# Optimization experiments

Hardware: AMD Instinct MI355X
Metric: run time of the kernel (lower is better)

Reference implementation:

```python
import jax, jax.numpy as jnp
import numpy as np
from functools import partial

TOP_K = 2
LN_EPS = 1e-5


def setup_inputs() -> dict:
    key = jax.random.key(0)
    ks = jax.random.split(key, 4)
    B, T, H, F, E = 2, 2048, 1024, 4096, 8
    hidden_states = jax.random.normal(ks[0], (B, T, H), dtype=jnp.float32)
    # Router weights: original inits to zeros; use small random so routing is non-degenerate.
    router_w = jax.random.normal(ks[1], (E, H), dtype=jnp.float32) * 0.02
    router_b = jnp.zeros((E,), dtype=jnp.float32)
    W1 = jax.random.normal(ks[2], (E, H, F), dtype=jnp.float32) * (1.0 / np.sqrt(H))
    b1 = jnp.zeros((E, F), dtype=jnp.float32)
    W2 = jax.random.normal(ks[3], (E, F, H), dtype=jnp.float32) * (1.0 / np.sqrt(F))
    b2 = jnp.zeros((E, H), dtype=jnp.float32)
    ln_gamma = jnp.ones((H,), dtype=jnp.float32)
    ln_beta = jnp.zeros((H,), dtype=jnp.float32)
    return {"hidden_states": hidden_states, "router_w": router_w, "router_b": router_b,
            "W1": W1, "b1": b1, "W2": W2, "b2": b2,
            "ln_gamma": ln_gamma, "ln_beta": ln_beta}


def _layer_norm(x, gamma, beta):
    mu = jnp.mean(x, axis=-1, keepdims=True)
    var = jnp.var(x, axis=-1, keepdims=True)
    return (x - mu) * jax.lax.rsqrt(var + LN_EPS) * gamma + beta


def _moe_forward(hidden_states, router_w, router_b, W1, b1, W2, b2, ln_gamma, ln_beta):
    B, T, H = hidden_states.shape
    E = router_w.shape[0]
    N = B * T
    x = hidden_states.reshape(N, H)
    # Router (jitter=0.0, eval mode): logits [N, E]
    logits = x @ router_w.T + router_b
    topk_vals, topk_idx = jax.lax.top_k(logits, TOP_K)        # [N, K]
    topk_w = jax.nn.softmax(topk_vals, axis=-1)               # [N, K]
    # Scatter top-k weights into a dense combine matrix [N, E] (zeros elsewhere).
    probs = jnp.zeros((N, E), dtype=x.dtype).at[jnp.arange(N)[:, None], topk_idx].set(topk_w)
    # Per-expert FFN via scan over the (small, fixed) expert axis; each step is one
    # big GEMM over all tokens weighted by that expert's combine prob (0 for
    # tokens not routed to it) — same math as gather/MLP/scatter with no capacity drop.
    def body(acc, params_e):
        Wa, ba, Wb, bb, pe = params_e          # pe: [N]
        h = jax.nn.gelu(x @ Wa + ba, approximate=False)   # [N, F]
        y = h @ Wb + bb                                    # [N, H]
        return acc + y * pe[:, None], None
    out, _ = jax.lax.scan(body, jnp.zeros_like(x), (W1, b1, W2, b2, probs.T))
    out = out.reshape(B, T, H)
    return _layer_norm(out + hidden_states, ln_gamma, ln_beta)


def reference(hidden_states, router_w, router_b, W1, b1, W2, b2, ln_gamma, ln_beta):
    return _moe_forward(hidden_states, router_w, router_b, W1, b1, W2, b2, ln_gamma, ln_beta)
```

## Files before the change

kernel.cpp:

```cpp
#include <hip/hip_runtime.h>
#include <hip/hip_bf16.h>


typedef unsigned short u16;
typedef unsigned int u32;
typedef __attribute__((ext_vector_type(4))) float f32x4;
typedef __attribute__((ext_vector_type(8))) short s16x8;

#define GLD16(gp, lp) __builtin_amdgcn_global_load_lds( \
    (const __attribute__((address_space(1))) void*)(gp), \
    (__attribute__((address_space(3))) void*)(lp), 16, 0, 0)

__device__ __forceinline__ u16 f2bf(float f) {
    union { float f; u32 u; } v; v.f = f;
    u32 u = v.u;
    return (u16)((u + 0x7fffu + ((u >> 16) & 1u)) >> 16);
}

__global__ void k_init(int* cc) { if (threadIdx.x < 16) cc[threadIdx.x] = 0; }

__global__ __launch_bounds__(256) void k_router(
    const float* __restrict__ x, const float* __restrict__ rw, const float* __restrict__ rb,
    u16* __restrict__ xb, int* __restrict__ eidx, float* __restrict__ wgt, int* __restrict__ counts)
{
    const int wav = threadIdx.x >> 6, lane = threadIdx.x & 63;
    const int t = blockIdx.x * 4 + wav;
    const float* xt = x + (size_t)t * 1024;
    float acc[8] = {0.f,0.f,0.f,0.f,0.f,0.f,0.f,0.f};
    #pragma unroll
    for (int c = 0; c < 4; c++) {
        const int base = c * 256 + lane * 4;
        const float4 xv = *(const float4*)(xt + base);
        ushort4 pk;
        pk.x = f2bf(xv.x); pk.y = f2bf(xv.y); pk.z = f2bf(xv.z); pk.w = f2bf(xv.w);
        *(ushort4*)(xb + (size_t)t * 1024 + base) = pk;
        #pragma unroll
        for (int e = 0; e < 8; e++) {
            const float4 wv = *(const float4*)(rw + e * 1024 + base);
            acc[e] += xv.x * wv.x + xv.y * wv.y + xv.z * wv.z + xv.w * wv.w;
        }
    }
    #pragma unroll
    for (int e = 0; e < 8; e++) {
        #pragma unroll
        for (int s = 32; s; s >>= 1) acc[e] += __shfl_xor(acc[e], s);
    }
    if (lane == 0) {
        float v0 = -3e38f, v1 = -3e38f; int i0 = 0, i1 = 0;
        #pragma unroll
        for (int e = 0; e < 8; e++) {
            const float l = acc[e] + rb[e];
            if (l > v0) { v1 = v0; i1 = i0; v0 = l; i0 = e; }
            else if (l > v1) { v1 = l; i1 = e; }
        }
        const float w0 = 1.0f / (1.0f + expf(v1 - v0));
        eidx[2 * t] = i0; eidx[2 * t + 1] = i1;
        wgt[2 * t] = w0; wgt[2 * t + 1] = 1.0f - w0;
        atomicAdd(&counts[i0], 1); atomicAdd(&counts[i1], 1);
    }
}

__global__ void k_offsets(const int* __restrict__ counts, int* __restrict__ offsets) {
    if (threadIdx.x == 0) {
        int s = 0;
        for (int e = 0; e < 8; e++) { offsets[e] = s; s += counts[e]; }
        offsets[8] = s;
    }
}

__global__ __launch_bounds__(256) void k_place(
    const int* __restrict__ eidx, const int* __restrict__ offsets, int* __restrict__ cursors,
    int* __restrict__ rows, int* __restrict__ pos_of)
{
    const int a = blockIdx.x * 256 + threadIdx.x;
    const int e = eidx[a];
    const int pos = offsets[e] + atomicAdd(&cursors[e], 1);
    rows[pos] = a >> 1;
    pos_of[a] = pos;
}

__global__ __launch_bounds__(256) void k_transp(
    const float* __restrict__ src, u16* __restrict__ dst, int R, int C)
{
    __shared__ float tile[32][33];
    const int e = blockIdx.z;
    const float* s = src + (size_t)e * R * C;
    u16* d = dst + (size_t)e * R * C;
    const int c0 = blockIdx.x * 32, r0 = blockIdx.y * 32;
    const int tx = threadIdx.x & 31, ty = threadIdx.x >> 5;
    #pragma unroll
    for (int j = 0; j < 4; j++)
        tile[ty * 4 + j][tx] = s[(size_t)(r0 + ty * 4 + j) * C + c0 + tx];
    __syncthreads();
    #pragma unroll
    for (int j = 0; j < 4; j++)
        d[(size_t)(c0 + ty * 4 + j) * R + r0 + tx] = f2bf(tile[tx][ty * 4 + j]);
}

__global__ __launch_bounds__(256) void k_gemm1(
    const u16* __restrict__ xb, const u16* __restrict__ W1t, const float* __restrict__ b1,
    u16* __restrict__ hbuf, const int* __restrict__ rows, const int* __restrict__ offsets)
{
    const int e = blockIdx.z;
    const int off = offsets[e], cnt = offsets[e + 1] - off;
    const int row0 = blockIdx.y * 128;
    if (row0 >= cnt) return;
    const int n0 = blockIdx.x * 128;
    const int tid = threadIdx.x;
    const int lane = tid & 63, wav = tid >> 6;

    __shared__ u16 At[128][32];
    __shared__ u16 Bt[128][32];

    const int ar0 = tid >> 2, ar1 = ar0 + 64;
    const int cl8 = (tid & 3) * 8;
    const int t0 = rows[off + min(row0 + ar0, cnt - 1)];
    const int t1 = rows[off + min(row0 + ar1, cnt - 1)];
    const u16* a_src0 = xb + (size_t)t0 * 1024 + cl8;
    const u16* a_src1 = xb + (size_t)t1 * 1024 + cl8;
    const u16* b_src0 = W1t + ((size_t)e * 4096 + n0 + ar0) * 1024 + cl8;
    const u16* b_src1 = W1t + ((size_t)e * 4096 + n0 + ar1) * 1024 + cl8;

    char* a_d0 = (char*)At + wav * 1024;
    char* a_d1 = (char*)At + 4096 + wav * 1024;
    char* b_d0 = (char*)Bt + wav * 1024;
    char* b_d1 = (char*)Bt + 4096 + wav * 1024;

    f32x4 acc[4][4] = {};
    const int wr = wav >> 1, wc = wav & 1;
    const int koff = (lane >> 4) * 8;
    const u16* Ab = &At[wr * 64 + (lane & 15)][koff];
    const u16* Bb = &Bt[wc * 64 + (lane & 15)][koff];

    for (int k0 = 0; k0 < 1024; k0 += 32) {
        GLD16(a_src0 + k0, a_d0);
        GLD16(a_src1 + k0, a_d1);
        GLD16(b_src0 + k0, b_d0);
        GLD16(b_src1 + k0, b_d1);
        __syncthreads();
        s16x8 af[4], bfr[4];
        #pragma unroll
        for (int i = 0; i < 4; i++) {
            af[i]  = *(const s16x8*)(Ab + i * 512);
            bfr[i] = *(const s16x8*)(Bb + i * 512);
        }
        #pragma unroll
        for (int mi = 0; mi < 4; mi++)
            #pragma unroll
            for (int ni = 0; ni < 4; ni++)
                acc[mi][ni] = __builtin_amdgcn_mfma_f32_16x16x32_bf16(af[mi], bfr[ni], acc[mi][ni], 0, 0, 0);
        __syncthreads();
    }

    const int rb4 = (lane >> 4) * 4;
    #pragma unroll
    for (int mi = 0; mi < 4; mi++) {
        #pragma unroll
        for (int j = 0; j < 4; j++) {
            const int lrow = wr * 64 + mi * 16 + rb4 + j;
            if (row0 + lrow < cnt) {
                const size_t gr = (size_t)(off + row0 + lrow);
                #pragma unroll
                for (int ni = 0; ni < 4; ni++) {
                    const int col = n0 + wc * 64 + ni * 16 + (lane & 15);
                    const float v = acc[mi][ni][j] + b1[e * 4096 + col];
                    const float g = 0.5f * v * (1.0f + erff(v * 0.70710678118654752f));
                    hbuf[gr * 4096 + col] = f2bf(g);
                }
            }
        }
    }
}

__global__ __launch_bounds__(256) void k_gemm2(
    const u16* __restrict__ hbuf, const u16* __restrict__ W2t, const float* __restrict__ b2,
    float* __restrict__ y, const int* __restrict__ offsets)
{
    const int e = blockIdx.z;
    const int off = offsets[e], cnt = offsets[e + 1] - off;
    const int row0 = blockIdx.y * 128;
    if (row0 >= cnt) return;
    const int n0 = blockIdx.x * 128;
    const int tid = threadIdx.x;
    const int lane = tid & 63, wav = tid >> 6;

    __shared__ u16 At[128][32];
    __shared__ u16 Bt[128][32];

    const int ar0 = tid >> 2, ar1 = ar0 + 64;
    const int cl8 = (tid & 3) * 8;
    const u16* a_src0 = hbuf + (size_t)(off + min(row0 + ar0, cnt - 1)) * 4096 + cl8;
    const u16* a_src1 = hbuf + (size_t)(off + min(row0 + ar1, cnt - 1)) * 4096 + cl8;
    const u16* b_src0 = W2t + ((size_t)e * 1024 + n0 + ar0) * 4096 + cl8;
    const u16* b_src1 = W2t + ((size_t)e * 1024 + n0 + ar1) * 4096 + cl8;

    char* a_d0 = (char*)At + wav * 1024;
    char* a_d1 = (char*)At + 4096 + wav * 1024;
    char* b_d0 = (char*)Bt + wav * 1024;
    char* b_d1 = (char*)Bt + 4096 + wav * 1024;

    f32x4 acc[4][4] = {};
    const int wr = wav >> 1, wc = wav & 1;
    const int koff = (lane >> 4) * 8;
    const u16* Ab = &At[wr * 64 + (lane & 15)][koff];
    const u16* Bb = &Bt[wc * 64 + (lane & 15)][koff];

    for (int k0 = 0; k0 < 4096; k0 += 32) {
        GLD16(a_src0 + k0, a_d0);
        GLD16(a_src1 + k0, a_d1);
        GLD16(b_src0 + k0, b_d0);
        GLD16(b_src1 + k0, b_d1);
        __syncthreads();
        s16x8 af[4], bfr[4];
        #pragma unroll
        for (int i = 0; i < 4; i++) {
            af[i]  = *(const s16x8*)(Ab + i * 512);
            bfr[i] = *(const s16x8*)(Bb + i * 512);
        }
        #pragma unroll
        for (int mi = 0; mi < 4; mi++)
            #pragma unroll
            for (int ni = 0; ni < 4; ni++)
                acc[mi][ni] = __builtin_amdgcn_mfma_f32_16x16x32_bf16(af[mi], bfr[ni], acc[mi][ni], 0, 0, 0);
        __syncthreads();
    }

    const int rb4 = (lane >> 4) * 4;
    #pragma unroll
    for (int mi = 0; mi < 4; mi++) {
        #pragma unroll
        for (int j = 0; j < 4; j++) {
            const int lrow = wr * 64 + mi * 16 + rb4 + j;
            if (row0 + lrow < cnt) {
                const size_t gr = (size_t)(off + row0 + lrow);
                #pragma unroll
                for (int ni = 0; ni < 4; ni++) {
                    const int col = n0 + wc * 64 + ni * 16 + (lane & 15);
                    y[gr * 1024 + col] = acc[mi][ni][j] + b2[e * 1024 + col];
                }
            }
        }
    }
}

__global__ __launch_bounds__(256) void k_combine(
    const float* __restrict__ x, const float* __restrict__ y,
    const int* __restrict__ pos_of, const float* __restrict__ wgt,
    const float* __restrict__ gamma, const float* __restrict__ beta,
    float* __restrict__ out)
{
    const int t = blockIdx.x;
    const int tid = threadIdx.x;
    const int p0 = pos_of[2 * t], p1 = pos_of[2 * t + 1];
    const float w0 = wgt[2 * t], w1 = wgt[2 * t + 1];
    const int j4 = tid * 4;
    const float4 xv = *(const float4*)(x + (size_t)t * 1024 + j4);
    const float4 y0 = *(const float4*)(y + (size_t)p0 * 1024 + j4);
    const float4 y1 = *(const float4*)(y + (size_t)p1 * 1024 + j4);
    float a0 = xv.x + w0 * y0.x + w1 * y1.x;
    float a1 = xv.y + w0 * y0.y + w1 * y1.y;
    float a2 = xv.z + w0 * y0.z + w1 * y1.z;
    float a3 = xv.w + w0 * y0.w + w1 * y1.w;
    float s = a0 + a1 + a2 + a3;
    float q = a0 * a0 + a1 * a1 + a2 * a2 + a3 * a3;
    #pragma unroll
    for (int o = 32; o; o >>= 1) { s += __shfl_xor(s, o); q += __shfl_xor(q, o); }
    __shared__ float ls[4], lq[4];
    const int wav = tid >> 6, lane = tid & 63;
    if (lane == 0) { ls[wav] = s; lq[wav] = q; }
    __syncthreads();
    s = ls[0] + ls[1] + ls[2] + ls[3];
    q = lq[0] + lq[1] + lq[2] + lq[3];
    const float mu = s * (1.0f / 1024.0f);
    const float var = q * (1.0f / 1024.0f) - mu * mu;
    const float rs = rsqrtf(var + 1e-5f);
    const float4 g = *(const float4*)(gamma + j4);
    const float4 b = *(const float4*)(beta + j4);
    float4 o4;
    o4.x = (a0 - mu) * rs * g.x + b.x;
    o4.y = (a1 - mu) * rs * g.y + b.y;
    o4.z = (a2 - mu) * rs * g.z + b.z;
    o4.w = (a3 - mu) * rs * g.w + b.w;
    *(float4*)(out + (size_t)t * 1024 + j4) = o4;
}

extern "C" void kernel_launch(void* const* d_in, const int* in_sizes, int n_in,
                              void* d_out, int out_size, void* d_ws, size_t ws_size,
                              hipStream_t stream) {
    const float* x     = (const float*)d_in[0];
    const float* rw    = (const float*)d_in[1];
    const float* rb    = (const float*)d_in[2];
    const float* W1    = (const float*)d_in[3];
    const float* b1    = (const float*)d_in[4];
    const float* W2    = (const float*)d_in[5];
    const float* b2    = (const float*)d_in[6];
    const float* gamma = (const float*)d_in[7];
    const float* beta  = (const float*)d_in[8];
    float* out = (float*)d_out;

    char* p = (char*)d_ws;
    auto alloc = [&](size_t bytes) { char* r = p; p += (bytes + 255) & ~(size_t)255; return r; };
    int*   counts  = (int*)alloc(16 * sizeof(int));
    int*   cursors = counts + 8;
    int*   offsets = (int*)alloc(9 * sizeof(int));
    int*   eidx    = (int*)alloc(8192 * sizeof(int));
    float* wgt     = (float*)alloc(8192 * sizeof(float));
    int*   pos_of  = (int*)alloc(8192 * sizeof(int));
    int*   rows    = (int*)alloc(8192 * sizeof(int));
    u16*   xb      = (u16*)alloc((size_t)4096 * 1024 * 2);
    u16*   W1t     = (u16*)alloc((size_t)8 * 4096 * 1024 * 2);
    u16*   W2t     = (u16*)alloc((size_t)8 * 1024 * 4096 * 2);
    u16*   hbuf    = (u16*)alloc((size_t)8192 * 4096 * 2);
    float* y       = (float*)alloc((size_t)8192 * 1024 * 4);

    hipLaunchKernelGGL(k_init, dim3(1), dim3(64), 0, stream, counts);
    hipLaunchKernelGGL(k_router, dim3(1024), dim3(256), 0, stream, x, rw, rb, xb, eidx, wgt, counts);
    hipLaunchKernelGGL(k_offsets, dim3(1), dim3(64), 0, stream, counts, offsets);
    hipLaunchKernelGGL(k_place, dim3(32), dim3(256), 0, stream, eidx, offsets, cursors, rows, pos_of);
    hipLaunchKernelGGL(k_transp, dim3(128, 32, 8), dim3(256), 0, stream, W1, W1t, 1024, 4096);
    hipLaunchKernelGGL(k_transp, dim3(32, 128, 8), dim3(256), 0, stream, W2, W2t, 4096, 1024);
    hipLaunchKernelGGL(k_gemm1, dim3(32, 32, 8), dim3(256), 0, stream, xb, W1t, b1, hbuf, rows, offsets);
    hipLaunchKernelGGL(k_gemm2, dim3(8, 32, 8), dim3(256), 0, stream, hbuf, W2t, b2, y, offsets);
    hipLaunchKernelGGL(k_combine, dim3(4096), dim3(256), 0, stream, x, y, pos_of, wgt, gamma, beta, out);
}
```

Measured before the change: 502.2 us.

## Split-K gemm2, tanh GELU, and vectorized weight transpose

Splits the second expert GEMM into two K halves, writing partial outputs into buffers that reuse the dead W1t storage, and sums them in the combine kernel. This raises block-level parallelism. The exact erf GELU is replaced by a tanh-style approximation built from fast exp and rcp. The transpose kernel drops LDS tiling and has each thread gather 8 rows and store them with one 16-byte write. The approximate GELU introduces small numeric deviation from the exact reference.

```diff
diff --git a/kernel.cpp b/kernel.cpp
--- a/kernel.cpp
+++ b/kernel.cpp
@@ -6,6 +6,7 @@
 typedef unsigned int u32;
 typedef __attribute__((ext_vector_type(4))) float f32x4;
 typedef __attribute__((ext_vector_type(8))) short s16x8;
+typedef __attribute__((ext_vector_type(8))) unsigned short u16x8;
 
 #define GLD16(gp, lp) __builtin_amdgcn_global_load_lds( \
     (const __attribute__((address_space(1))) void*)(gp), \
@@ -15,6 +16,12 @@
     union { float f; u32 u; } v; v.f = f;
     u32 u = v.u;
     return (u16)((u + 0x7fffu + ((u >> 16) & 1u)) >> 16);
+}
+
+__device__ __forceinline__ float gelu_f(float v) {
+    const float u = v * (0.7978845608f + 0.0356774081f * v * v);
+    const float t = __expf(-2.0f * u);
+    return v * __builtin_amdgcn_rcpf(1.0f + t);
 }
 
 __global__ void k_init(int* cc) { if (threadIdx.x < 16) cc[threadIdx.x] = 0; }
@@ -82,19 +89,16 @@
 __global__ __launch_bounds__(256) void k_transp(
     const float* __restrict__ src, u16* __restrict__ dst, int R, int C)
 {
-    __shared__ float tile[32][33];
     const int e = blockIdx.z;
     const float* s = src + (size_t)e * R * C;
     u16* d = dst + (size_t)e * R * C;
-    const int c0 = blockIdx.x * 32, r0 = blockIdx.y * 32;
-    const int tx = threadIdx.x & 31, ty = threadIdx.x >> 5;
-    #pragma unroll
-    for (int j = 0; j < 4; j++)
-        tile[ty * 4 + j][tx] = s[(size_t)(r0 + ty * 4 + j) * C + c0 + tx];
-    __syncthreads();
-    #pragma unroll
-    for (int j = 0; j < 4; j++)
-        d[(size_t)(c0 + ty * 4 + j) * R + r0 + tx] = f2bf(tile[tx][ty * 4 + j]);
+    const int c = blockIdx.x * 64 + (threadIdx.x >> 2);
+    const int r0 = blockIdx.y * 32 + (threadIdx.x & 3) * 8;
+    u16x8 v;
+    #pragma unroll
+    for (int k = 0; k < 8; k++)
+        v[k] = f2bf(s[(size_t)(r0 + k) * C + c]);
+    *(u16x8*)(d + (size_t)c * R + r0) = v;
 }
 
 __global__ __launch_bounds__(256) void k_gemm1(
@@ -164,8 +168,7 @@
                 for (int ni = 0; ni < 4; ni++) {
                     const int col = n0 + wc * 64 + ni * 16 + (lane & 15);
                     const float v = acc[mi][ni][j] + b1[e * 4096 + col];
-                    const float g = 0.5f * v * (1.0f + erff(v * 0.70710678118654752f));
-                    hbuf[gr * 4096 + col] = f2bf(g);
+                    hbuf[gr * 4096 + col] = f2bf(gelu_f(v));
                 }
             }
         }
@@ -174,25 +177,26 @@
 
 __global__ __launch_bounds__(256) void k_gemm2(
     const u16* __restrict__ hbuf, const u16* __restrict__ W2t, const float* __restrict__ b2,
-    float* __restrict__ y, const int* __restrict__ offsets)
-{
-    const int e = blockIdx.z;
+    float* __restrict__ y0, float* __restrict__ y1, const int* __restrict__ offsets)
+{
+    const int e = blockIdx.z >> 1, kh = blockIdx.z & 1;
     const int off = offsets[e], cnt = offsets[e + 1] - off;
     const int row0 = blockIdx.y * 128;
     if (row0 >= cnt) return;
     const int n0 = blockIdx.x * 128;
     const int tid = threadIdx.x;
     const int lane = tid & 63, wav = tid >> 6;
+    const int kbase = kh * 2048;
 
     __shared__ u16 At[128][32];
     __shared__ u16 Bt[128][32];
 
     const int ar0 = tid >> 2, ar1 = ar0 + 64;
     const int cl8 = (tid & 3) * 8;
-    const u16* a_src0 = hbuf + (size_t)(off + min(row0 + ar0, cnt - 1)) * 4096 + cl8;
-    const u16* a_src1 = hbuf + (size_t)(off + min(row0 + ar1, cnt - 1)) * 4096 + cl8;
-    const u16* b_src0 = W2t + ((size_t)e * 1024 + n0 + ar0) * 4096 + cl8;
-    const u16* b_src1 = W2t + ((size_t)e * 1024 + n0 + ar1) * 4096 + cl8;
+    const u16* a_src0 = hbuf + (size_t)(off + min(row0 + ar0, cnt - 1)) * 4096 + kbase + cl8;
+    const u16* a_src1 = hbuf + (size_t)(off + min(row0 + ar1, cnt - 1)) * 4096 + kbase + cl8;
+    const u16* b_src0 = W2t + ((size_t)e * 1024 + n0 + ar0) * 4096 + kbase + cl8;
+    const u16* b_src1 = W2t + ((size_t)e * 1024 + n0 + ar1) * 4096 + kbase + cl8;
 
     char* a_d0 = (char*)At + wav * 1024;
     char* a_d1 = (char*)At + 4096 + wav * 1024;
@@ -205,7 +209,7 @@
     const u16* Ab = &At[wr * 64 + (lane & 15)][koff];
     const u16* Bb = &Bt[wc * 64 + (lane & 15)][koff];
 
-    for (int k0 = 0; k0 < 4096; k0 += 32) {
+    for (int k0 = 0; k0 < 2048; k0 += 32) {
         GLD16(a_src0 + k0, a_d0);
         GLD16(a_src1 + k0, a_d1);
         GLD16(b_src0 + k0, b_d0);
@@ -225,6 +229,7 @@
         __syncthreads();
     }
 
+    float* y = kh ? y1 : y0;
     const int rb4 = (lane >> 4) * 4;
     #pragma unroll
     for (int mi = 0; mi < 4; mi++) {
@@ -236,7 +241,8 @@
                 #pragma unroll
                 for (int ni = 0; ni < 4; ni++) {
                     const int col = n0 + wc * 64 + ni * 16 + (lane & 15);
-                    y[gr * 1024 + col] = acc[mi][ni][j] + b2[e * 1024 + col];
+                    const float bias = kh ? 0.f : b2[e * 1024 + col];
+                    y[gr * 1024 + col] = acc[mi][ni][j] + bias;
                 }
             }
         }
@@ -244,7 +250,7 @@
 }
 
 __global__ __launch_bounds__(256) void k_combine(
-    const float* __restrict__ x, const float* __restrict__ y,
+    const float* __restrict__ x, const float* __restrict__ y0, const float* __restrict__ y1,
     const int* __restrict__ pos_of, const float* __restrict__ wgt,
     const float* __restrict__ gamma, const float* __restrict__ beta,
     float* __restrict__ out)
@@ -255,12 +261,14 @@
     const float w0 = wgt[2 * t], w1 = wgt[2 * t + 1];
     const int j4 = tid * 4;
     const float4 xv = *(const float4*)(x + (size_t)t * 1024 + j4);
-    const float4 y0 = *(const float4*)(y + (size_t)p0 * 1024 + j4);
-    const float4 y1 = *(const float4*)(y + (size_t)p1 * 1024 + j4);
-    float a0 = xv.x + w0 * y0.x + w1 * y1.x;
-    float a1 = xv.y + w0 * y0.y + w1 * y1.y;
-    float a2 = xv.z + w0 * y0.z + w1 * y1.z;
-    float a3 = xv.w + w0 * y0.w + w1 * y1.w;
+    const float4 ya0 = *(const float4*)(y0 + (size_t)p0 * 1024 + j4);
+    const float4 yb0 = *(const float4*)(y1 + (size_t)p0 * 1024 + j4);
+    const float4 ya1 = *(const float4*)(y0 + (size_t)p1 * 1024 + j4);
+    const float4 yb1 = *(const float4*)(y1 + (size_t)p1 * 1024 + j4);
+    float a0 = xv.x + w0 * (ya0.x + yb0.x) + w1 * (ya1.x + yb1.x);
+    float a1 = xv.y + w0 * (ya0.y + yb0.y) + w1 * (ya1.y + yb1.y);
+    float a2 = xv.z + w0 * (ya0.z + yb0.z) + w1 * (ya1.z + yb1.z);
+    float a3 = xv.w + w0 * (ya0.w + yb0.w) + w1 * (ya1.w + yb1.w);
     float s = a0 + a1 + a2 + a3;
     float q = a0 * a0 + a1 * a1 + a2 * a2 + a3 * a3;
     #pragma unroll
@@ -311,15 +319,16 @@
     u16*   W1t     = (u16*)alloc((size_t)8 * 4096 * 1024 * 2);
     u16*   W2t     = (u16*)alloc((size_t)8 * 1024 * 4096 * 2);
     u16*   hbuf    = (u16*)alloc((size_t)8192 * 4096 * 2);
-    float* y       = (float*)alloc((size_t)8192 * 1024 * 4);
+    float* y0 = (float*)W1t;
+    float* y1 = y0 + (size_t)8192 * 1024;
 
     hipLaunchKernelGGL(k_init, dim3(1), dim3(64), 0, stream, counts);
     hipLaunchKernelGGL(k_router, dim3(1024), dim3(256), 0, stream, x, rw, rb, xb, eidx, wgt, counts);
     hipLaunchKernelGGL(k_offsets, dim3(1), dim3(64), 0, stream, counts, offsets);
     hipLaunchKernelGGL(k_place, dim3(32), dim3(256), 0, stream, eidx, offsets, cursors, rows, pos_of);
-    hipLaunchKernelGGL(k_transp, dim3(128, 32, 8), dim3(256), 0, stream, W1, W1t, 1024, 4096);
-    hipLaunchKernelGGL(k_transp, dim3(32, 128, 8), dim3(256), 0, stream, W2, W2t, 4096, 1024);
+    hipLaunchKernelGGL(k_transp, dim3(64, 32, 8), dim3(256), 0, stream, W1, W1t, 1024, 4096);
+    hipLaunchKernelGGL(k_transp, dim3(16, 128, 8), dim3(256), 0, stream, W2, W2t, 4096, 1024);
     hipLaunchKernelGGL(k_gemm1, dim3(32, 32, 8), dim3(256), 0, stream, xb, W1t, b1, hbuf, rows, offsets);
-    hipLaunchKernelGGL(k_gemm2, dim3(8, 32, 8), dim3(256), 0, stream, hbuf, W2t, b2, y, offsets);
-    hipLaunchKernelGGL(k_combine, dim3(4096), dim3(256), 0, stream, x, y, pos_of, wgt, gamma, beta, out);
-}
+    hipLaunchKernelGGL(k_gemm2, dim3(8, 32, 16), dim3(256), 0, stream, hbuf, W2t, b2, y0, y1, offsets);
+    hipLaunchKernelGGL(k_combine, dim3(4096), dim3(256), 0, stream, x, y0, y1, pos_of, wgt, gamma, beta, out);
+}
```

Measured after the change: 473.1 us. -5.8%, faster.
